# Performance work log

Hardware: AMD Instinct MI355X
Metric: run time of the kernel (lower is better)

Reference implementation:

```python
import jax, jax.numpy as jnp
import numpy as np

NUM_HEADS = 8
TEMPERATURE = 10000.0


def sine_embed(pos, dim):
    """Sine positional embedding of 2D offsets. pos [..., 2] -> [..., dim]."""
    half = dim // 2  # dims per coordinate
    dim_t = TEMPERATURE ** (2.0 * (jnp.arange(half) // 2).astype(jnp.float32) / half)
    s = pos[..., :, None] / dim_t  # [..., 2, half]
    emb = jnp.stack([jnp.sin(s[..., 0::2]), jnp.cos(s[..., 1::2])], axis=-1)
    emb = emb.reshape(s.shape[:-1] + (half,))  # interleaved sin/cos per coord
    return emb.reshape(pos.shape[:-1] + (dim,))


def setup_inputs() -> dict:
    key = jax.random.key(0)
    ks = jax.random.split(key, 16)
    N, H, W, C, K = 2, 40, 40, 256, 100
    h = NUM_HEADS
    sc = 1.0 / np.sqrt(C)
    return {
        "query_feature": jax.random.normal(ks[0], (N, H, W, C), jnp.float32),
        "query_position": jax.random.uniform(ks[1], (N, H, W, 2), jnp.float32),
        "key_feature": jax.random.normal(ks[2], (N, K, C), jnp.float32),
        "key_position": jax.random.uniform(ks[3], (N, K, 2), jnp.float32),
        # MultiheadAttention params (torch convention: weight [out, in])
        "in_proj_w": jax.random.normal(ks[4], (3 * C, C), jnp.float32) * sc,
        "in_proj_b": jnp.zeros((3 * C,), jnp.float32),
        "out_proj_w": jax.random.normal(ks[5], (C, C), jnp.float32) * sc,
        "out_proj_b": jnp.zeros((C,), jnp.float32),
        # PositionalEncodingSineLearned MLP: sine(C) -> C -> num_heads
        "pos_w1": jax.random.normal(ks[6], (C, C), jnp.float32) * sc,
        "pos_b1": jnp.zeros((C,), jnp.float32),
        "pos_w2": jax.random.normal(ks[7], (h, C), jnp.float32) * sc,
        "pos_b2": jnp.zeros((h,), jnp.float32),
        # cat_pos branch params
        "pos_trans_w": jax.random.normal(ks[8], (2, 2), jnp.float32),
        "embed_w": jax.random.normal(ks[9], (C, C + 2), jnp.float32) * 0.01,
        "embed_b": jnp.zeros((C,), jnp.float32),
    }


def reference(query_feature, query_position, key_feature, key_position,
              in_proj_w, in_proj_b, out_proj_w, out_proj_b,
              pos_w1, pos_b1, pos_w2, pos_b2,
              pos_trans_w, embed_w, embed_b):
    N, H, W, C = query_feature.shape
    h = NUM_HEADS
    d = C // h
    q = query_feature.reshape(N, -1, C)            # [N,Q,C]
    qp = query_position.reshape(N, -1, 2)          # [N,Q,2] (scale_terms = 1.0)
    Q = q.shape[1]
    K = key_feature.shape[1]

    # pairwise relative positions: [N,Q,K,2]
    rel_pos = key_position[:, None, :, :] - qp[:, :, None, :]

    # learned sine relative positional encoding -> per-head additive bias
    pe = sine_embed(rel_pos, C)                              # [N,Q,K,C]
    hid = jax.nn.relu(pe @ pos_w1.T + pos_b1)                # [N,Q,K,C]
    bias = (hid @ pos_w2.T + pos_b2).transpose(0, 3, 1, 2)   # [N,h,Q,K]

    # multihead attention with additive relative bias
    wq, wk, wv = jnp.split(in_proj_w, 3, axis=0)
    bq, bk, bv = jnp.split(in_proj_b, 3, axis=0)
    qh = ((q @ wq.T + bq).reshape(N, Q, h, d)) * (d ** -0.5)
    kh = (key_feature @ wk.T + bk).reshape(N, K, h, d)
    vh = (key_feature @ wv.T + bv).reshape(N, K, h, d)
    scores = jnp.einsum('nqhd,nkhd->nhqk', qh, kh) + bias
    attn = jax.nn.softmax(scores, axis=-1)                   # [N,h,Q,K]
    ctx = jnp.einsum('nhqk,nkhd->nqhd', attn, vh).reshape(N, Q, C)
    refined = ctx @ out_proj_w.T + out_proj_b                # [N,Q,C]

    # cat_pos: attention-weighted relative position aggregation
    attn_w = attn.mean(axis=1)                               # [N,Q,K]
    new_rel = jnp.einsum('nqk,nqkc->nqc', attn_w, jax.lax.stop_gradient(rel_pos))
    new_pos = new_rel @ pos_trans_w.T                        # [N,Q,2]

    feat = jax.nn.relu(q + refined)
    feat = jax.nn.relu(jnp.concatenate([feat, new_pos], axis=-1) @ embed_w.T + embed_b)
    return feat.reshape(N, H, W, C)
```

## Files before the change

kernel.cpp:

```cpp
#include <hip/hip_runtime.h>
#include <math.h>

typedef __bf16 bf16x8 __attribute__((ext_vector_type(8)));
typedef __bf16 bf16x4 __attribute__((ext_vector_type(4)));
typedef float  f32x4  __attribute__((ext_vector_type(4)));


#define WS_KH    0u
#define WS_VH    51200u
#define WS_EWP   102400u
#define WS_QHB   168960u
#define WS_BIASB 578560u
#define WS_KEB   2012160u
#define WS_W1B   2038560u
#define WS_W2PB  2071328u

__device__ __forceinline__ float rdlane(float v, int l) {
  return __uint_as_float(__builtin_amdgcn_readlane(__float_as_uint(v), l));
}

__global__ __launch_bounds__(256, 2) void prep_kernel(
    const float* __restrict__ qfeat, const float* __restrict__ kfeat,
    const float* __restrict__ kpos,
    const float* __restrict__ ipw, const float* __restrict__ ipb,
    const float* __restrict__ pos_w1, const float* __restrict__ pos_w2,
    const float* __restrict__ embed_w, float* __restrict__ ws)
{
  __shared__ float x[8 * 256];
  int bid = blockIdx.x, t = threadIdx.x;

  if (bid < 50) {
    int r = bid * 4 + (t >> 6);
    int u = t & 63;
    float p0 = kpos[r * 2 + 0], p1 = kpos[r * 2 + 1];
    __bf16* keb = (__bf16*)(ws + WS_KEB);
    bf16x4 o;
#pragma unroll
    for (int j = 0; j < 4; j++) {
      int col = u * 4 + j;
      int c = col >> 7, i = (col & 127) >> 1;
      float p = c ? p1 : p0;
      float inv = exp2f((float)i * (-13.287712379549449f / 64.0f));
      float v = p * inv;
      o[j] = (__bf16)((col & 1) ? __cosf(v) : __sinf(v));
    }
    *(bf16x4*)(keb + r * 264 + u * 4) = o;
  } else if (bid < 114) {
    int idx = (bid - 50) * 1024 + t * 4;
    float4 v = *(const float4*)(pos_w1 + idx);
    bf16x4 o; o[0] = (__bf16)v.x; o[1] = (__bf16)v.y; o[2] = (__bf16)v.z; o[3] = (__bf16)v.w;
    *(bf16x4*)((__bf16*)(ws + WS_W1B) + idx) = o;
  } else if (bid == 114) {
    __bf16* w2pb = (__bf16*)(ws + WS_W2PB);
    for (int i = 0; i < 16; i++) {
      int idx = t * 16 + i;
      w2pb[idx] = (idx < 2048) ? (__bf16)pos_w2[idx] : (__bf16)0.0f;
    }
  } else if (bid < 147) {
    int r0 = (bid - 115) * 8;
    for (int rr = 0; rr < 8; rr++) {
      int r = r0 + rr;
      for (int j = t; j < 260; j += 256)
        ws[WS_EWP + r * 260 + j] = (j < 258) ? embed_w[r * 258 + j] : 0.0f;
    }
  } else if (bid < 547) {
    int r0 = (bid - 147) * 8;
    for (int i = t; i < 2048; i += 256) x[i] = qfeat[(unsigned)r0 * 256u + i];
    __syncthreads();
    float acc[8]; float bq = ipb[t];
#pragma unroll
    for (int rr = 0; rr < 8; rr++) acc[rr] = bq;
    const float* wrow = ipw + (unsigned)t * 256u;
    for (int j = 0; j < 256; j += 4) {
      float4 w4 = *(const float4*)(wrow + j);
#pragma unroll
      for (int rr = 0; rr < 8; rr++) {
        float4 x4 = *(const float4*)(x + rr * 256 + j);
        acc[rr] = fmaf(x4.x, w4.x, fmaf(x4.y, w4.y, fmaf(x4.z, w4.z, fmaf(x4.w, w4.w, acc[rr]))));
      }
    }
    __bf16* qhb = (__bf16*)(ws + WS_QHB);
#pragma unroll
    for (int rr = 0; rr < 8; rr++)
      qhb[(unsigned)(r0 + rr) * 256u + t] = (__bf16)(acc[rr] * 0.17677669529663687f);
  } else {
    int b2 = bid - 547; int n = b2 >> 4, tile = b2 & 15;
    int r0l = tile * 7; int cnt = 100 - r0l; if (cnt > 7) cnt = 7; if (cnt <= 0) return;
    int r0 = n * 100 + r0l;
    for (int i = t; i < cnt * 256; i += 256) x[i] = kfeat[(unsigned)r0 * 256u + i];
    __syncthreads();
    float ak[7], av[7]; float bk = ipb[256 + t], bv = ipb[512 + t];
#pragma unroll
    for (int rr = 0; rr < 7; rr++) { ak[rr] = bk; av[rr] = bv; }
    const float* wkr = ipw + (unsigned)(256 + t) * 256u;
    const float* wvr = ipw + (unsigned)(512 + t) * 256u;
    for (int j = 0; j < 256; j += 4) {
      float4 wk4 = *(const float4*)(wkr + j);
      float4 wv4 = *(const float4*)(wvr + j);
#pragma unroll
      for (int rr = 0; rr < 7; rr++) {
        float4 x4 = *(const float4*)(x + rr * 256 + j);
        ak[rr] = fmaf(x4.x, wk4.x, fmaf(x4.y, wk4.y, fmaf(x4.z, wk4.z, fmaf(x4.w, wk4.w, ak[rr]))));
        av[rr] = fmaf(x4.x, wv4.x, fmaf(x4.y, wv4.y, fmaf(x4.z, wv4.z, fmaf(x4.w, wv4.w, av[rr]))));
      }
    }
    for (int rr = 0; rr < 7; rr++) {
      if (rr < cnt) {
        ws[WS_KH + (unsigned)(r0 + rr) * 256u + t] = ak[rr];
        ws[WS_VH + (unsigned)(r0 + rr) * 256u + t] = av[rr];
      }
    }
  }
}

__global__ __launch_bounds__(512) void bias_kernel(
    const float* __restrict__ qpos,
    const float* __restrict__ pos_b1, const float* __restrict__ pos_b2,
    float* __restrict__ ws)
{
  __shared__ __align__(16) char smem[63488];
  __bf16* qe_s   = (__bf16*)(smem + 28672);
  __bf16* region = (__bf16*)(smem + 30720);

  int bid = blockIdx.x;
  int n = bid / 400;
  int q0 = bid * 4;
  int t = threadIdx.x;
  int lane = t & 63, w = t >> 6;
  int l15 = lane & 15, quad = lane >> 4;

  const __bf16* keb = (const __bf16*)(ws + WS_KEB) + (unsigned)(n * 100) * 264u;
  const __bf16* w1b = (const __bf16*)(ws + WS_W1B);
  const __bf16* w2pb = (const __bf16*)(ws + WS_W2PB);
  __bf16* biasb = (__bf16*)(ws + WS_BIASB);

  {
    int idx = t * 2;
    int q = idx >> 8, u = idx & 255;
    int c = u >> 7, i = (u & 127) >> 1;
    float p = qpos[(q0 + q) * 2 + c];
    float inv = exp2f((float)i * (-13.287712379549449f / 64.0f));
    float v = p * inv;
    qe_s[idx]     = (__bf16)__sinf(v);
    qe_s[idx + 1] = (__bf16)__cosf(v);
  }

  bf16x8 wfrag[2][8];
#pragma unroll
  for (int ct = 0; ct < 2; ct++)
#pragma unroll
    for (int kc = 0; kc < 8; kc++)
      wfrag[ct][kc] = *(const bf16x8*)(w1b + (unsigned)(w * 32 + ct * 16 + l15) * 256u + kc * 32 + quad * 8);
  float b1v[2][4];
#pragma unroll
  for (int ct = 0; ct < 2; ct++)
#pragma unroll
    for (int r = 0; r < 4; r++) b1v[ct][r] = pos_b1[w * 32 + ct * 16 + quad * 4 + r];
  float b2v[4];
#pragma unroll
  for (int r = 0; r < 4; r++) b2v[r] = pos_b2[(quad * 4 + r) & 7];

  auto gen = [&](int q, int pair, int buf) {
    if (t < 448) {
      int key = t >> 2, sub = t & 3;
      int cb = pair * 64 + sub * 16;
      bf16x8 fr0, fr1;
      const __bf16* qp = qe_s + q * 256 + cb;
      bf16x8 q0f = *(const bf16x8*)qp;
      bf16x8 q1f = *(const bf16x8*)(qp + 8);
      if (key < 100) {
        const __bf16* kp = keb + (unsigned)key * 264u + cb;
        bf16x8 k0f = *(const bf16x8*)kp;
        bf16x8 k1f = *(const bf16x8*)(kp + 8);
#pragma unroll
        for (int jj = 0; jj < 4; jj++) {
          float sk = (float)k0f[2 * jj], ck = (float)k0f[2 * jj + 1];
          float sq = (float)q0f[2 * jj], cq = (float)q0f[2 * jj + 1];
          fr0[2 * jj]     = (__bf16)(sk * cq - ck * sq);
          fr0[2 * jj + 1] = (__bf16)(ck * cq + sk * sq);
          float sk1 = (float)k1f[2 * jj], ck1 = (float)k1f[2 * jj + 1];
          float sq1 = (float)q1f[2 * jj], cq1 = (float)q1f[2 * jj + 1];
          fr1[2 * jj]     = (__bf16)(sk1 * cq1 - ck1 * sq1);
          fr1[2 * jj + 1] = (__bf16)(ck1 * cq1 + sk1 * sq1);
        }
      } else {
#pragma unroll
        for (int jj = 0; jj < 8; jj++) { fr0[jj] = (__bf16)0.f; fr1[jj] = (__bf16)0.f; }
      }
      int mt = key >> 4, kl = key & 15;
      int kcl = sub >> 1;
      int qd0 = (sub & 1) * 2;
      bf16x8* base = (bf16x8*)smem + buf * 896 + kcl * 448 + mt * 64;
      base[qd0 * 16 + (kl ^ (qd0 * 2 + kcl))]             = fr0;
      base[(qd0 + 1) * 16 + (kl ^ (qd0 * 2 + 2 + kcl))]   = fr1;
    }
  };

  f32x4 zero4; zero4[0] = 0.f; zero4[1] = 0.f; zero4[2] = 0.f; zero4[3] = 0.f;

  __syncthreads();
  gen(0, 0, 0);
  __syncthreads();

  for (int q = 0; q < 4; q++) {
    f32x4 acc[2][7];
#pragma unroll
    for (int ct = 0; ct < 2; ct++)
#pragma unroll
      for (int mt = 0; mt < 7; mt++) acc[ct][mt] = zero4;

    for (int p = 0; p < 4; p++) {
      if (p < 3) gen(q, p + 1, (p + 1) & 1);
      else if (q < 3) gen(q + 1, 0, 0);
      const bf16x8* pb = (const bf16x8*)smem + (p & 1) * 896;
#pragma unroll
      for (int kh = 0; kh < 2; kh++) {
        int kc = p * 2 + kh;
        bf16x8 pf[7];
#pragma unroll
        for (int mt = 0; mt < 7; mt++)
          pf[mt] = pb[kh * 448 + mt * 64 + quad * 16 + (l15 ^ (quad * 2 + kh))];
#pragma unroll
        for (int mt = 0; mt < 7; mt++) {
          acc[0][mt] = __builtin_amdgcn_mfma_f32_16x16x32_bf16(wfrag[0][kc], pf[mt], acc[0][mt], 0, 0, 0);
          acc[1][mt] = __builtin_amdgcn_mfma_f32_16x16x32_bf16(wfrag[1][kc], pf[mt], acc[1][mt], 0, 0, 0);
        }
      }
      __syncthreads();
    }

#pragma unroll
    for (int ct = 0; ct < 2; ct++)
#pragma unroll
      for (int mt = 0; mt < 7; mt++)
#pragma unroll
        for (int r = 0; r < 4; r++)
          acc[ct][mt][r] = fmaxf(acc[ct][mt][r] + b1v[ct][r], 0.0f);

    auto wreg = [&](int mt, int slot) {
#pragma unroll
      for (int ct = 0; ct < 2; ct++) {
        int qt = ct * 2 + (quad >> 1);
        int j0 = (quad & 1) * 4;
        bf16x4 o;
#pragma unroll
        for (int r = 0; r < 4; r++) o[r] = (__bf16)acc[ct][mt][r];
        *(bf16x4*)(region + slot * 4096 + ((w * 64 + qt * 16 + l15) << 3) + j0) = o;
      }
    };
    auto g2 = [&](int mt, int slot) {
      f32x4 acc2 = zero4;
      const bf16x8* rg = (const bf16x8*)(region + slot * 4096);
#pragma unroll
      for (int s = 0; s < 8; s++) {
        bf16x8 w2f = *(const bf16x8*)(w2pb + (unsigned)l15 * 256u + s * 32 + quad * 8);
        bf16x8 hf = rg[s * 64 + lane];
        acc2 = __builtin_amdgcn_mfma_f32_16x16x32_bf16(w2f, hf, acc2, 0, 0, 0);
      }
      if (quad < 2) {
        bf16x4 o;
#pragma unroll
        for (int r = 0; r < 4; r++) o[r] = (__bf16)(acc2[r] + b2v[r]);
        *(bf16x4*)(biasb + ((unsigned)(q0 + q) * 112u + mt * 16 + l15) * 8u + quad * 4) = o;
      }
    };

    wreg(0, 0); wreg(1, 1); wreg(2, 2); wreg(3, 3);
    __syncthreads();
    if (w < 4) g2(w, w);
    __syncthreads();
    wreg(4, 0); wreg(5, 1); wreg(6, 2);
    __syncthreads();
    if (w < 3) g2(4 + w, w);
  }
}

__global__ __launch_bounds__(256, 4) void attn_kernel(
    const float* __restrict__ qfeat, const float* __restrict__ qpos,
    const float* __restrict__ kpos,
    const float* __restrict__ out_w, const float* __restrict__ out_b,
    const float* __restrict__ embed_b, const float* __restrict__ ptw,
    const float* __restrict__ ws, float* __restrict__ out)
{
  __shared__ float qh_s[4 * 8 * 36];
  __shared__ float attn_s[4 * 8 * 116];
  __shared__ float ctx_s[4 * 264];
  __shared__ float cat_s[4 * 264];
  __shared__ float aw_s[4 * 104];

  int bid = blockIdx.x;
  int qg0 = bid * 4;
  int n = bid / 400;
  int t = threadIdx.x;

  const __bf16* qhb = (const __bf16*)(ws + WS_QHB);
  const __bf16* biasb = (const __bf16*)(ws + WS_BIASB);
  const float* kh = ws + WS_KH;
  const float* vh = ws + WS_VH;
  const float* ewp = ws + WS_EWP;

  for (int i = t; i < 1024; i += 256) {
    int q = i >> 8, c = i & 255;
    qh_s[(q * 8 + (c >> 5)) * 36 + (c & 31)] = (float)qhb[(unsigned)(qg0 + q) * 256u + c];
  }
  __syncthreads();

  for (int i = 0; i < 4; i++) {
    int p = t + i * 256;
    if (p < 800) {
      int k = p >> 3, h = p & 7;
      const float4* kf = (const float4*)(kh + (unsigned)(n * 100 + k) * 256u + h * 32);
      float4 kv[8];
#pragma unroll
      for (int dd = 0; dd < 8; dd++) kv[dd] = kf[dd];
#pragma unroll
      for (int q = 0; q < 4; q++) {
        const float4* qf = (const float4*)(qh_s + (q * 8 + h) * 36);
        float s = (float)biasb[((unsigned)(qg0 + q) * 112u + k) * 8u + h];
#pragma unroll
        for (int dd = 0; dd < 8; dd++) {
          float4 qv = qf[dd];
          s += kv[dd].x * qv.x + kv[dd].y * qv.y + kv[dd].z * qv.z + kv[dd].w * qv.w;
        }
        attn_s[(q * 8 + h) * 116 + k] = s;
      }
    }
  }
  __syncthreads();

  {
    int q = t >> 6, h = (t >> 3) & 7, j = t & 7;
    float* row = attn_s + (q * 8 + h) * 116;
    float mx = -1e30f;
    for (int k = j; k < 100; k += 8) mx = fmaxf(mx, row[k]);
    mx = fmaxf(mx, __shfl_xor(mx, 1, 8));
    mx = fmaxf(mx, __shfl_xor(mx, 2, 8));
    mx = fmaxf(mx, __shfl_xor(mx, 4, 8));
    float sum = 0.f;
    for (int k = j; k < 100; k += 8) { float e = __expf(row[k] - mx); row[k] = e; sum += e; }
    sum += __shfl_xor(sum, 1, 8);
    sum += __shfl_xor(sum, 2, 8);
    sum += __shfl_xor(sum, 4, 8);
    float inv = 1.0f / sum;
    for (int k = j; k < 100; k += 8) row[k] *= inv;
  }
  __syncthreads();

  for (int p = t; p < 416; p += 256) {
    int q = p / 104, k = p % 104;
    if (k < 100) {
      float s = 0.f;
#pragma unroll
      for (int h = 0; h < 8; h++) s += attn_s[(q * 8 + h) * 116 + k];
      aw_s[q * 104 + k] = s * 0.125f;
    }
  }
  {
    int c = t, h = c >> 5;
    float a0 = 0.f, a1 = 0.f, a2 = 0.f, a3 = 0.f;
    const float* vp = vh + (unsigned)(n * 100) * 256u + c;
    const float* r0 = attn_s + (0 * 8 + h) * 116;
    const float* r1 = attn_s + (1 * 8 + h) * 116;
    const float* r2 = attn_s + (2 * 8 + h) * 116;
    const float* r3 = attn_s + (3 * 8 + h) * 116;
#pragma unroll 4
    for (int k = 0; k < 100; k++) {
      float vv = vp[(unsigned)k * 256u];
      a0 = fmaf(r0[k], vv, a0);
      a1 = fmaf(r1[k], vv, a1);
      a2 = fmaf(r2[k], vv, a2);
      a3 = fmaf(r3[k], vv, a3);
    }
    ctx_s[0 * 264 + c] = a0; ctx_s[1 * 264 + c] = a1;
    ctx_s[2 * 264 + c] = a2; ctx_s[3 * 264 + c] = a3;
  }
  __syncthreads();

  if (t < 8) {
    int q = t >> 1, cd = t & 1;
    float qp = qpos[(qg0 + q) * 2 + cd];
    float s = 0.f;
    for (int k = 0; k < 100; k++)
      s = fmaf(aw_s[q * 104 + k], kpos[(n * 100 + k) * 2 + cd] - qp, s);
    float so = __shfl_xor(s, 1, 2);
    if (cd == 0) cat_s[q * 264 + 256] = ptw[0] * s + ptw[1] * so;
    else         cat_s[q * 264 + 257] = ptw[2] * so + ptw[3] * s;
  }

  {
    int c = t, lane = t & 63;
    float ob = out_b[c];
    float acc0 = ob, acc1 = ob, acc2 = ob, acc3 = ob;
    const float* wr = out_w + (unsigned)c * 256u;
    for (int ch = 0; ch < 4; ch++) {
      float v0 = ctx_s[0 * 264 + ch * 64 + lane];
      float v1 = ctx_s[1 * 264 + ch * 64 + lane];
      float v2 = ctx_s[2 * 264 + ch * 64 + lane];
      float v3 = ctx_s[3 * 264 + ch * 64 + lane];
      const float* wp = wr + ch * 64;
#pragma unroll 4
      for (int j4 = 0; j4 < 16; j4++) {
        float4 w4 = *(const float4*)(wp + j4 * 4);
        int jb = j4 * 4;
        acc0 = fmaf(rdlane(v0, jb + 0), w4.x, acc0);
        acc1 = fmaf(rdlane(v1, jb + 0), w4.x, acc1);
        acc2 = fmaf(rdlane(v2, jb + 0), w4.x, acc2);
        acc3 = fmaf(rdlane(v3, jb + 0), w4.x, acc3);
        acc0 = fmaf(rdlane(v0, jb + 1), w4.y, acc0);
        acc1 = fmaf(rdlane(v1, jb + 1), w4.y, acc1);
        acc2 = fmaf(rdlane(v2, jb + 1), w4.y, acc2);
        acc3 = fmaf(rdlane(v3, jb + 1), w4.y, acc3);
        acc0 = fmaf(rdlane(v0, jb + 2), w4.z, acc0);
        acc1 = fmaf(rdlane(v1, jb + 2), w4.z, acc1);
        acc2 = fmaf(rdlane(v2, jb + 2), w4.z, acc2);
        acc3 = fmaf(rdlane(v3, jb + 2), w4.z, acc3);
        acc0 = fmaf(rdlane(v0, jb + 3), w4.w, acc0);
        acc1 = fmaf(rdlane(v1, jb + 3), w4.w, acc1);
        acc2 = fmaf(rdlane(v2, jb + 3), w4.w, acc2);
        acc3 = fmaf(rdlane(v3, jb + 3), w4.w, acc3);
      }
    }
    cat_s[0 * 264 + c] = fmaxf(qfeat[(unsigned)(qg0 + 0) * 256u + c] + acc0, 0.f);
    cat_s[1 * 264 + c] = fmaxf(qfeat[(unsigned)(qg0 + 1) * 256u + c] + acc1, 0.f);
    cat_s[2 * 264 + c] = fmaxf(qfeat[(unsigned)(qg0 + 2) * 256u + c] + acc2, 0.f);
    cat_s[3 * 264 + c] = fmaxf(qfeat[(unsigned)(qg0 + 3) * 256u + c] + acc3, 0.f);
  }
  __syncthreads();

  {
    int c = t, lane = t & 63;
    float eb = embed_b[c];
    float acc0 = eb, acc1 = eb, acc2 = eb, acc3 = eb;
    const float* er = ewp + (unsigned)c * 260u;
    for (int ch = 0; ch < 4; ch++) {
      float v0 = cat_s[0 * 264 + ch * 64 + lane];
      float v1 = cat_s[1 * 264 + ch * 64 + lane];
      float v2 = cat_s[2 * 264 + ch * 64 + lane];
      float v3 = cat_s[3 * 264 + ch * 64 + lane];
      const float* wp = er + ch * 64;
#pragma unroll 4
      for (int j4 = 0; j4 < 16; j4++) {
        float4 w4 = *(const float4*)(wp + j4 * 4);
        int jb = j4 * 4;
        acc0 = fmaf(rdlane(v0, jb + 0), w4.x, acc0);
        acc1 = fmaf(rdlane(v1, jb + 0), w4.x, acc1);
        acc2 = fmaf(rdlane(v2, jb + 0), w4.x, acc2);
        acc3 = fmaf(rdlane(v3, jb + 0), w4.x, acc3);
        acc0 = fmaf(rdlane(v0, jb + 1), w4.y, acc0);
        acc1 = fmaf(rdlane(v1, jb + 1), w4.y, acc1);
        acc2 = fmaf(rdlane(v2, jb + 1), w4.y, acc2);
        acc3 = fmaf(rdlane(v3, jb + 1), w4.y, acc3);
        acc0 = fmaf(rdlane(v0, jb + 2), w4.z, acc0);
        acc1 = fmaf(rdlane(v1, jb + 2), w4.z, acc1);
        acc2 = fmaf(rdlane(v2, jb + 2), w4.z, acc2);
        acc3 = fmaf(rdlane(v3, jb + 2), w4.z, acc3);
        acc0 = fmaf(rdlane(v0, jb + 3), w4.w, acc0);
        acc1 = fmaf(rdlane(v1, jb + 3), w4.w, acc1);
        acc2 = fmaf(rdlane(v2, jb + 3), w4.w, acc2);
        acc3 = fmaf(rdlane(v3, jb + 3), w4.w, acc3);
      }
    }
    float4 wt = *(const float4*)(er + 256);
    acc0 += cat_s[0 * 264 + 256] * wt.x + cat_s[0 * 264 + 257] * wt.y;
    acc1 += cat_s[1 * 264 + 256] * wt.x + cat_s[1 * 264 + 257] * wt.y;
    acc2 += cat_s[2 * 264 + 256] * wt.x + cat_s[2 * 264 + 257] * wt.y;
    acc3 += cat_s[3 * 264 + 256] * wt.x + cat_s[3 * 264 + 257] * wt.y;
    out[(unsigned)(qg0 + 0) * 256u + c] = fmaxf(acc0, 0.f);
    out[(unsigned)(qg0 + 1) * 256u + c] = fmaxf(acc1, 0.f);
    out[(unsigned)(qg0 + 2) * 256u + c] = fmaxf(acc2, 0.f);
    out[(unsigned)(qg0 + 3) * 256u + c] = fmaxf(acc3, 0.f);
  }
}

extern "C" void kernel_launch(void* const* d_in, const int* in_sizes, int n_in,
                              void* d_out, int out_size, void* d_ws, size_t ws_size,
                              hipStream_t stream)
{
  const float* query_feature  = (const float*)d_in[0];
  const float* query_position = (const float*)d_in[1];
  const float* key_feature    = (const float*)d_in[2];
  const float* key_position   = (const float*)d_in[3];
  const float* in_proj_w      = (const float*)d_in[4];
  const float* in_proj_b      = (const float*)d_in[5];
  const float* out_proj_w     = (const float*)d_in[6];
  const float* out_proj_b     = (const float*)d_in[7];
  const float* pos_w1         = (const float*)d_in[8];
  const float* pos_b1         = (const float*)d_in[9];
  const float* pos_w2         = (const float*)d_in[10];
  const float* pos_b2         = (const float*)d_in[11];
  const float* pos_trans_w    = (const float*)d_in[12];
  const float* embed_w        = (const float*)d_in[13];
  const float* embed_b        = (const float*)d_in[14];
  float* ws  = (float*)d_ws;
  float* out = (float*)d_out;

  hipLaunchKernelGGL(prep_kernel, dim3(579), dim3(256), 0, stream,
                     query_feature, key_feature, key_position,
                     in_proj_w, in_proj_b, pos_w1, pos_w2, embed_w, ws);
  hipLaunchKernelGGL(bias_kernel, dim3(800), dim3(512), 0, stream,
                     query_position, pos_b1, pos_b2, ws);
  hipLaunchKernelGGL(attn_kernel, dim3(800), dim3(256), 0, stream,
                     query_feature, query_position, key_position,
                     out_proj_w, out_proj_b, embed_b, pos_trans_w,
                     ws, out);
}
```

Baseline: 294.5 us.

## Restructure bias kernel second GEMM via shuffles and LDS atomics for occupancy

The bias kernel no longer keeps all W1 fragments resident in registers. It reloads two k-chunks per pipeline step and requests 4 blocks per CU. The second MLP layer (hidden -> heads) now builds MFMA operands with cross-lane shuffles instead of staging through an LDS region. Each wave computes a partial product over its 32 hidden channels and accumulates it with LDS float atomics into a double-buffered reduction array, which is flushed one query later. This cuts LDS from about 62KB and drops several barriers, at the cost of extra global loads of W1, shuffle instructions, and atomic contention in shared memory.

```diff
diff --git a/kernel.cpp b/kernel.cpp
--- a/kernel.cpp
+++ b/kernel.cpp
@@ -17,6 +17,12 @@
 
 __device__ __forceinline__ float rdlane(float v, int l) {
   return __uint_as_float(__builtin_amdgcn_readlane(__float_as_uint(v), l));
+}
+
+__device__ __forceinline__ unsigned packbf(float a, float b) {
+  unsigned short ua = __builtin_bit_cast(unsigned short, (__bf16)a);
+  unsigned short ub = __builtin_bit_cast(unsigned short, (__bf16)b);
+  return (unsigned)ua | ((unsigned)ub << 16);
 }
 
 __global__ __launch_bounds__(256, 2) void prep_kernel(
@@ -113,14 +119,14 @@
   }
 }
 
-__global__ __launch_bounds__(512) void bias_kernel(
+__global__ __launch_bounds__(512, 4) void bias_kernel(
     const float* __restrict__ qpos,
     const float* __restrict__ pos_b1, const float* __restrict__ pos_b2,
     float* __restrict__ ws)
 {
-  __shared__ __align__(16) char smem[63488];
-  __bf16* qe_s   = (__bf16*)(smem + 28672);
-  __bf16* region = (__bf16*)(smem + 30720);
+  __shared__ __align__(16) char smem[30720];
+  __shared__ float red_s[2][896];
+  __bf16* qe_s = (__bf16*)(smem + 28672);
 
   int bid = blockIdx.x;
   int n = bid / 400;
@@ -133,6 +139,8 @@
   const __bf16* w1b = (const __bf16*)(ws + WS_W1B);
   const __bf16* w2pb = (const __bf16*)(ws + WS_W2PB);
   __bf16* biasb = (__bf16*)(ws + WS_BIASB);
+
+  for (int i = t; i < 1792; i += 512) ((float*)red_s)[i] = 0.f;
 
   {
     int idx = t * 2;
@@ -145,20 +153,7 @@
     qe_s[idx + 1] = (__bf16)__cosf(v);
   }
 
-  bf16x8 wfrag[2][8];
-#pragma unroll
-  for (int ct = 0; ct < 2; ct++)
-#pragma unroll
-    for (int kc = 0; kc < 8; kc++)
-      wfrag[ct][kc] = *(const bf16x8*)(w1b + (unsigned)(w * 32 + ct * 16 + l15) * 256u + kc * 32 + quad * 8);
-  float b1v[2][4];
-#pragma unroll
-  for (int ct = 0; ct < 2; ct++)
-#pragma unroll
-    for (int r = 0; r < 4; r++) b1v[ct][r] = pos_b1[w * 32 + ct * 16 + quad * 4 + r];
-  float b2v[4];
-#pragma unroll
-  for (int r = 0; r < 4; r++) b2v[r] = pos_b2[(quad * 4 + r) & 7];
+  bf16x8 w2f = *(const bf16x8*)(w2pb + (unsigned)l15 * 256u + w * 32 + quad * 8);
 
   auto gen = [&](int q, int pair, int buf) {
     if (t < 448) {
@@ -210,68 +205,90 @@
       for (int mt = 0; mt < 7; mt++) acc[ct][mt] = zero4;
 
     for (int p = 0; p < 4; p++) {
+      bf16x8 wf[2][2];
+#pragma unroll
+      for (int ct = 0; ct < 2; ct++) {
+        const __bf16* wr = w1b + (unsigned)(w * 32 + ct * 16 + l15) * 256u + p * 64 + quad * 8;
+        wf[0][ct] = *(const bf16x8*)wr;
+        wf[1][ct] = *(const bf16x8*)(wr + 32);
+      }
+
       if (p < 3) gen(q, p + 1, (p + 1) & 1);
       else if (q < 3) gen(q + 1, 0, 0);
-      const bf16x8* pb = (const bf16x8*)smem + (p & 1) * 896;
+
+      if (p == 0 && q > 0) {
+        int pb_ = (q - 1) & 1;
+        for (int i2 = t; i2 < 896; i2 += 512) {
+          int key = i2 >> 3, h = i2 & 7;
+          float v = red_s[pb_][i2] + pos_b2[h];
+          biasb[((unsigned)(q0 + q - 1) * 112u + key) * 8u + h] = (__bf16)v;
+          red_s[pb_][i2] = 0.f;
+        }
+      }
+
+      const bf16x8* pbuf = (const bf16x8*)smem + (p & 1) * 896;
 #pragma unroll
       for (int kh = 0; kh < 2; kh++) {
-        int kc = p * 2 + kh;
-        bf16x8 pf[7];
+#pragma unroll
+        for (int mt = 0; mt < 7; mt++) {
+          bf16x8 pf = pbuf[kh * 448 + mt * 64 + quad * 16 + (l15 ^ (quad * 2 + kh))];
+          acc[0][mt] = __builtin_amdgcn_mfma_f32_16x16x32_bf16(wf[kh][0], pf, acc[0][mt], 0, 0, 0);
+          acc[1][mt] = __builtin_amdgcn_mfma_f32_16x16x32_bf16(wf[kh][1], pf, acc[1][mt], 0, 0, 0);
+        }
+      }
+      __syncthreads();
+    }
+
+    {
+      float b1a[2][4];
+#pragma unroll
+      for (int ct = 0; ct < 2; ct++)
+#pragma unroll
+        for (int r = 0; r < 4; r++) b1a[ct][r] = pos_b1[w * 32 + ct * 16 + quad * 4 + r];
+#pragma unroll
+      for (int ct = 0; ct < 2; ct++)
 #pragma unroll
         for (int mt = 0; mt < 7; mt++)
-          pf[mt] = pb[kh * 448 + mt * 64 + quad * 16 + (l15 ^ (quad * 2 + kh))];
-#pragma unroll
-        for (int mt = 0; mt < 7; mt++) {
-          acc[0][mt] = __builtin_amdgcn_mfma_f32_16x16x32_bf16(wfrag[0][kc], pf[mt], acc[0][mt], 0, 0, 0);
-          acc[1][mt] = __builtin_amdgcn_mfma_f32_16x16x32_bf16(wfrag[1][kc], pf[mt], acc[1][mt], 0, 0, 0);
+#pragma unroll
+          for (int r = 0; r < 4; r++)
+            acc[ct][mt][r] = fmaxf(acc[ct][mt][r] + b1a[ct][r], 0.0f);
+    }
+
+    {
+      int qa = (quad & 1) * 2;
+      int s0 = qa * 16 + l15, s1 = s0 + 16;
+      bool hi = (quad >= 2);
+      int rb = q & 1;
+#pragma unroll
+      for (int mt = 0; mt < 7; mt++) {
+        unsigned a0 = packbf(acc[0][mt][0], acc[0][mt][1]);
+        unsigned a1 = packbf(acc[0][mt][2], acc[0][mt][3]);
+        unsigned b0 = packbf(acc[1][mt][0], acc[1][mt][1]);
+        unsigned b1_ = packbf(acc[1][mt][2], acc[1][mt][3]);
+        unsigned w0a = __shfl(a0, s0), w1a = __shfl(a1, s0);
+        unsigned w2a = __shfl(a0, s1), w3a = __shfl(a1, s1);
+        unsigned w0b = __shfl(b0, s0), w1b_ = __shfl(b1_, s0);
+        unsigned w2b = __shfl(b0, s1), w3b = __shfl(b1_, s1);
+        union { unsigned u[4]; bf16x8 v; } fb;
+        fb.u[0] = hi ? w0b : w0a;
+        fb.u[1] = hi ? w1b_ : w1a;
+        fb.u[2] = hi ? w2b : w2a;
+        fb.u[3] = hi ? w3b : w3a;
+        f32x4 d2 = __builtin_amdgcn_mfma_f32_16x16x32_bf16(fb.v, w2f, zero4, 0, 0, 0);
+        if (l15 < 8) {
+#pragma unroll
+          for (int r = 0; r < 4; r++)
+            atomicAdd(&red_s[rb][(mt * 16 + quad * 4 + r) * 8 + l15], d2[r]);
         }
       }
-      __syncthreads();
-    }
-
-#pragma unroll
-    for (int ct = 0; ct < 2; ct++)
-#pragma unroll
-      for (int mt = 0; mt < 7; mt++)
-#pragma unroll
-        for (int r = 0; r < 4; r++)
-          acc[ct][mt][r] = fmaxf(acc[ct][mt][r] + b1v[ct][r], 0.0f);
-
-    auto wreg = [&](int mt, int slot) {
-#pragma unroll
-      for (int ct = 0; ct < 2; ct++) {
-        int qt = ct * 2 + (quad >> 1);
-        int j0 = (quad & 1) * 4;
-        bf16x4 o;
-#pragma unroll
-        for (int r = 0; r < 4; r++) o[r] = (__bf16)acc[ct][mt][r];
-        *(bf16x4*)(region + slot * 4096 + ((w * 64 + qt * 16 + l15) << 3) + j0) = o;
-      }
-    };
-    auto g2 = [&](int mt, int slot) {
-      f32x4 acc2 = zero4;
-      const bf16x8* rg = (const bf16x8*)(region + slot * 4096);
-#pragma unroll
-      for (int s = 0; s < 8; s++) {
-        bf16x8 w2f = *(const bf16x8*)(w2pb + (unsigned)l15 * 256u + s * 32 + quad * 8);
-        bf16x8 hf = rg[s * 64 + lane];
-        acc2 = __builtin_amdgcn_mfma_f32_16x16x32_bf16(w2f, hf, acc2, 0, 0, 0);
-      }
-      if (quad < 2) {
-        bf16x4 o;
-#pragma unroll
-        for (int r = 0; r < 4; r++) o[r] = (__bf16)(acc2[r] + b2v[r]);
-        *(bf16x4*)(biasb + ((unsigned)(q0 + q) * 112u + mt * 16 + l15) * 8u + quad * 4) = o;
-      }
-    };
-
-    wreg(0, 0); wreg(1, 1); wreg(2, 2); wreg(3, 3);
+    }
     __syncthreads();
-    if (w < 4) g2(w, w);
-    __syncthreads();
-    wreg(4, 0); wreg(5, 1); wreg(6, 2);
-    __syncthreads();
-    if (w < 3) g2(4 + w, w);
+  }
+
+  for (int i2 = t; i2 < 896; i2 += 512) {
+    int key = i2 >> 3, h = i2 & 7;
+    float v = red_s[1][i2] + pos_b2[h];
+    biasb[((unsigned)(q0 + 3) * 112u + key) * 8u + h] = (__bf16)v;
   }
 }
 
```

New measurement: 446.3 us. 1.52x slower.
